# Performance work log

Hardware: AMD Instinct MI355X
Metric: run time of the kernel (lower is better)

The kernel has to match this reference:

```python
import jax, jax.numpy as jnp
import numpy as np

N = 100000      # nodes
E = 1600000     # edges (avg degree 16)
IN, H, EMB = 64, 128, 64
G = 64          # graphs in the batch


def _w(key, shape, fan_in):
    return jax.random.normal(key, shape, jnp.float32) * (1.0 / np.sqrt(fan_in))


def setup_inputs() -> dict:
    key = jax.random.key(0)
    ks = jax.random.split(key, 16)
    x = jax.random.normal(ks[0], (N, IN), jnp.float32)
    edge_index = jax.random.randint(ks[1], (2, E), 0, N, dtype=jnp.int64)
    batch = jnp.sort(jax.random.randint(ks[2], (N,), 0, G, dtype=jnp.int64))
    return {
        "x": x,
        "edge_index": edge_index,
        "batch": batch,
        # SAGEConv 1: lin_l acts on aggregated neighbors, lin_r on the root node
        "Wl1": _w(ks[3], (IN, H), IN), "Wr1": _w(ks[4], (IN, H), IN), "b1": jnp.zeros((H,), jnp.float32),
        "Wl2": _w(ks[5], (H, H), H), "Wr2": _w(ks[6], (H, H), H), "b2": jnp.zeros((H,), jnp.float32),
        "Wl3": _w(ks[7], (H, H), H), "Wr3": _w(ks[8], (H, H), H), "b3": jnp.zeros((H,), jnp.float32),
        "W_lin1": _w(ks[9], (H, H // 2), H), "b_lin1": jnp.zeros((H // 2,), jnp.float32),
        "W_lin2": _w(ks[10], (H // 2, EMB), H // 2), "b_lin2": jnp.zeros((EMB,), jnp.float32),
    }


def _sage_conv(x, src, dst, Wl, Wr, b):
    # mean-aggregate source features onto destination nodes
    msg_sum = jax.ops.segment_sum(x[src], dst, num_segments=N)          # [N, d]
    deg = jax.ops.segment_sum(jnp.ones((src.shape[0],), x.dtype), dst, num_segments=N)
    mean = msg_sum / jnp.clip(deg, 1.0)[:, None]
    return mean @ Wl + x @ Wr + b


def _forward(x, edge_index, batch,
             Wl1, Wr1, b1, Wl2, Wr2, b2, Wl3, Wr3, b3,
             W_lin1, b_lin1, W_lin2, b_lin2):
    src, dst = edge_index[0], edge_index[1]
    h = jax.nn.relu(_sage_conv(x, src, dst, Wl1, Wr1, b1))
    h = jax.nn.relu(_sage_conv(h, src, dst, Wl2, Wr2, b2))
    h = jax.nn.relu(_sage_conv(h, src, dst, Wl3, Wr3, b3))
    # global mean pool per graph
    pooled = jax.ops.segment_sum(h, batch, num_segments=G)              # [G, H]
    counts = jax.ops.segment_sum(jnp.ones((N,), h.dtype), batch, num_segments=G)
    pooled = pooled / jnp.clip(counts, 1.0)[:, None]
    h = jax.nn.relu(pooled @ W_lin1 + b_lin1)
    # dropout p=0.5 is identity in eval mode
    return h @ W_lin2 + b_lin2


def reference(x, edge_index, batch,
              Wl1, Wr1, b1, Wl2, Wr2, b2, Wl3, Wr3, b3,
              W_lin1, b_lin1, W_lin2, b_lin2):
    return _forward(x, edge_index, batch, Wl1, Wr1, b1, Wl2, Wr2, b2,
                    Wl3, Wr3, b3, W_lin1, b_lin1, W_lin2, b_lin2)
```

## Files before the change

kernel.cpp:

```cpp
#include <hip/hip_runtime.h>
#include <hip/hip_bf16.h>
#include <cstdint>
#include <cstddef>

#define NN 100000
#define NE 1600000
#define NG 64
#define NPAD 100096
#define NBUK 782
#define CAP 3072
#define NFB 256
#define CHUNK 6250

typedef short short8v __attribute__((ext_vector_type(8)));
typedef float float4v __attribute__((ext_vector_type(4)));


__device__ __forceinline__ int lower_bound_i(const int* __restrict__ a, int n, int v) {
  int lo = 0, hi = n;
  while (lo < hi) { int m = (lo + hi) >> 1; if (a[m] < v) lo = m + 1; else hi = m; }
  return lo;
}

__device__ __forceinline__ float bf2f(ushort u) {
  return __uint_as_float(((unsigned int)u) << 16);
}

__device__ __forceinline__ float bflo(unsigned int u) {
  return __uint_as_float(u << 16);
}
__device__ __forceinline__ float bfhi(unsigned int u) {
  return __uint_as_float(u & 0xffff0000u);
}

__device__ __forceinline__ ushort f2bf(float f) {
  __hip_bfloat16 h = __float2bfloat16(f);
  return *reinterpret_cast<ushort*>(&h);
}


__global__ void pack_x_kernel(const float* __restrict__ x, ushort* __restrict__ xb,
                              int* __restrict__ bcur) {
  int i4 = blockIdx.x * blockDim.x + threadIdx.x;
  if (i4 < NBUK) bcur[i4] = i4 * CAP;
  int idx = i4 * 4;
  if (idx >= NN * 64) return;
  float4 v = *(const float4*)(x + idx);
  ushort4 o;
  o.x = f2bf(v.x); o.y = f2bf(v.y); o.z = f2bf(v.z); o.w = f2bf(v.w);
  *(ushort4*)(xb + idx) = o;
}

__device__ __forceinline__ void pack_one(const float* __restrict__ Wl,
                                         const float* __restrict__ Wr,
                                         ushort* __restrict__ Wp, int K, int idx) {
  int lane = idx & 63;
  int ft   = (idx >> 6) & 7;
  int kkp  = idx >> 9;
  int kbase = kkp * 32 + (lane >> 4) * 8;
  int isR = kbase >= K;
  const float* W = isR ? Wr : Wl;
  int k0 = kbase - (isR ? K : 0);
  int colf = ft * 16 + (lane & 15);
  ushort4 lo, hi;
  lo.x = f2bf(W[(k0 + 0) * 128 + colf]);
  lo.y = f2bf(W[(k0 + 1) * 128 + colf]);
  lo.z = f2bf(W[(k0 + 2) * 128 + colf]);
  lo.w = f2bf(W[(k0 + 3) * 128 + colf]);
  hi.x = f2bf(W[(k0 + 4) * 128 + colf]);
  hi.y = f2bf(W[(k0 + 5) * 128 + colf]);
  hi.z = f2bf(W[(k0 + 6) * 128 + colf]);
  hi.w = f2bf(W[(k0 + 7) * 128 + colf]);
  *(ushort4*)(Wp + (size_t)idx * 8)     = lo;
  *(ushort4*)(Wp + (size_t)idx * 8 + 4) = hi;
}

__global__ void pack_w_all_kernel(const float* __restrict__ Wl1, const float* __restrict__ Wr1,
                                  ushort* __restrict__ wp1,
                                  const float* __restrict__ Wl2, const float* __restrict__ Wr2,
                                  ushort* __restrict__ wp2,
                                  const float* __restrict__ Wl3, const float* __restrict__ Wr3,
                                  ushort* __restrict__ wp3) {
  int idx = blockIdx.x * blockDim.x + threadIdx.x;
  if (idx < 2048)       pack_one(Wl1, Wr1, wp1, 64,  idx);
  else if (idx < 6144)  pack_one(Wl2, Wr2, wp2, 128, idx - 2048);
  else if (idx < 10240) pack_one(Wl3, Wr3, wp3, 128, idx - 6144);
}


__global__ __launch_bounds__(256) void bucket_fill_kernel(const int* __restrict__ src,
                                                          const int* __restrict__ dst,
                                                          int* __restrict__ bcur,
                                                          unsigned int* __restrict__ bp) {
  __shared__ int lhist[NBUK];
  __shared__ int lbase[NBUK];
  int tid = threadIdx.x;
  int e0 = blockIdx.x * CHUNK;
  int e1 = e0 + CHUNK;
  for (int i = tid; i < NBUK; i += 256) lhist[i] = 0;
  __syncthreads();
  for (int i = e0 + tid; i < e1; i += 256) atomicAdd(&lhist[dst[i] >> 7], 1);
  __syncthreads();
  for (int b = tid; b < NBUK; b += 256) {
    int c = lhist[b];
    lbase[b] = c ? atomicAdd(&bcur[b], c) : 0;
    lhist[b] = 0;
  }
  __syncthreads();
  for (int i = e0 + tid; i < e1; i += 256) {
    int d = dst[i];
    int b = d >> 7;
    int p = atomicAdd(&lhist[b], 1);
    int pos = lbase[b] + p;
    if (pos < (b + 1) * CAP)
      bp[pos] = ((unsigned int)(d & 127) << 17) | (unsigned int)src[i];
  }
}

__global__ __launch_bounds__(1024) void bucket_scan_kernel(const int* __restrict__ bcur,
                                                           int* __restrict__ boff,
                                                           int* __restrict__ rs,
                                                           float* __restrict__ pooled) {
  __shared__ int wsum[16];
  int tid = threadIdx.x, lane = tid & 63, wid = tid >> 6;
  int v = 0;
  if (tid < NBUK) v = min(bcur[tid] - tid * CAP, CAP);
  int incl = v;
  #pragma unroll
  for (int off = 1; off < 64; off <<= 1) {
    int t = __shfl_up(incl, off, 64);
    if (lane >= off) incl += t;
  }
  if (lane == 63) wsum[wid] = incl;
  __syncthreads();
  if (tid == 0) {
    int acc = 0;
    #pragma unroll
    for (int j = 0; j < 16; ++j) { int t = wsum[j]; wsum[j] = acc; acc += t; }
  }
  __syncthreads();
  int excl = incl - v + wsum[wid];
  if (tid <= NBUK) boff[tid] = excl;
  for (int i = tid; i < NG * 128; i += 1024) pooled[i] = 0.f;
  if (tid == 0) rs[NN] = NE;
}

__global__ __launch_bounds__(256) void bucket_csr_kernel(const unsigned int* __restrict__ bp,
                                                         const int* __restrict__ boff,
                                                         int* __restrict__ rs,
                                                         int* __restrict__ col) {
  __shared__ int sdeg[128], sinc[128], lcur[128];
  int b = blockIdx.x, tid = threadIdx.x;
  int n0 = b << 7;
  int e0 = boff[b], e1 = boff[b + 1];
  int cnt = e1 - e0;
  const unsigned int* __restrict__ mybp = bp + (size_t)b * CAP;
  if (tid < 128) sdeg[tid] = 0;
  __syncthreads();
  for (int i = tid; i < cnt; i += 256) atomicAdd(&sdeg[mybp[i] >> 17], 1);
  __syncthreads();
  if (tid < 128) sinc[tid] = sdeg[tid];
  __syncthreads();
  #pragma unroll
  for (int off = 1; off < 128; off <<= 1) {
    int add = 0;
    if (tid < 128 && tid >= off) add = sinc[tid - off];
    __syncthreads();
    if (tid < 128) sinc[tid] += add;
    __syncthreads();
  }
  if (tid < 128) {
    int excl = sinc[tid] - sdeg[tid];
    lcur[tid] = excl;
    int node = n0 + tid;
    if (node < NN) rs[node] = e0 + excl;
  }
  __syncthreads();
  for (int i = tid; i < cnt; i += 256) {
    unsigned int v = mybp[i];
    int p = atomicAdd(&lcur[v >> 17], 1);
    col[e0 + p] = (int)(v & 0x1FFFF);
  }
}


__global__ __launch_bounds__(256) void agg64_kernel(const unsigned int* __restrict__ X,
                                                    const int* __restrict__ rs,
                                                    const int* __restrict__ col,
                                                    unsigned int* __restrict__ out, int n) {
  int lane = threadIdx.x & 63;
  int node = blockIdx.x * 4 + (threadIdx.x >> 6);
  if (node >= n) return;
  int a = rs[node], b = rs[node + 1];
  int grp = lane >> 3, fl = lane & 7;
  float acc[8];
  #pragma unroll
  for (int j = 0; j < 8; ++j) acc[j] = 0.f;
  for (int jb = a; jb < b; jb += 64) {
    int v = (jb + lane < b) ? col[jb + lane] : 0;
    int cnt = min(64, b - jb);
    for (int t = 0; t < cnt; t += 8) {
      int idx = t + grp;
      int s = __shfl(v, min(idx, cnt - 1), 64);
      uint4 u = *(const uint4*)(X + (size_t)s * 32 + fl * 4);
      if (idx < cnt) {
        acc[0] += bflo(u.x); acc[1] += bfhi(u.x);
        acc[2] += bflo(u.y); acc[3] += bfhi(u.y);
        acc[4] += bflo(u.z); acc[5] += bfhi(u.z);
        acc[6] += bflo(u.w); acc[7] += bfhi(u.w);
      }
    }
  }
  #pragma unroll
  for (int off = 8; off <= 32; off <<= 1)
    #pragma unroll
    for (int j = 0; j < 8; ++j) acc[j] += __shfl_xor(acc[j], off, 64);
  int d = b - a;
  float inv = d > 0 ? 1.0f / (float)d : 0.f;
  if (grp == 0) {
    uint4 o;
    o.x = (unsigned int)f2bf(acc[0] * inv) | ((unsigned int)f2bf(acc[1] * inv) << 16);
    o.y = (unsigned int)f2bf(acc[2] * inv) | ((unsigned int)f2bf(acc[3] * inv) << 16);
    o.z = (unsigned int)f2bf(acc[4] * inv) | ((unsigned int)f2bf(acc[5] * inv) << 16);
    o.w = (unsigned int)f2bf(acc[6] * inv) | ((unsigned int)f2bf(acc[7] * inv) << 16);
    *(uint4*)(out + (size_t)node * 32 + fl * 4) = o;
  }
}

__global__ __launch_bounds__(256) void agg128_kernel(const unsigned int* __restrict__ X,
                                                     const int* __restrict__ rs,
                                                     const int* __restrict__ col,
                                                     unsigned int* __restrict__ out, int n) {
  int lane = threadIdx.x & 63;
  int node = blockIdx.x * 4 + (threadIdx.x >> 6);
  if (node >= n) return;
  int a = rs[node], b = rs[node + 1];
  int grp = lane >> 4, fl = lane & 15;
  float acc[8];
  #pragma unroll
  for (int j = 0; j < 8; ++j) acc[j] = 0.f;
  for (int jb = a; jb < b; jb += 64) {
    int v = (jb + lane < b) ? col[jb + lane] : 0;
    int cnt = min(64, b - jb);
    for (int t = 0; t < cnt; t += 4) {
      int idx = t + grp;
      int s = __shfl(v, min(idx, cnt - 1), 64);
      uint4 u = *(const uint4*)(X + (size_t)s * 64 + fl * 4);
      if (idx < cnt) {
        acc[0] += bflo(u.x); acc[1] += bfhi(u.x);
        acc[2] += bflo(u.y); acc[3] += bfhi(u.y);
        acc[4] += bflo(u.z); acc[5] += bfhi(u.z);
        acc[6] += bflo(u.w); acc[7] += bfhi(u.w);
      }
    }
  }
  #pragma unroll
  for (int off = 16; off <= 32; off <<= 1)
    #pragma unroll
    for (int j = 0; j < 8; ++j) acc[j] += __shfl_xor(acc[j], off, 64);
  int d = b - a;
  float inv = d > 0 ? 1.0f / (float)d : 0.f;
  if (grp == 0) {
    uint4 o;
    o.x = (unsigned int)f2bf(acc[0] * inv) | ((unsigned int)f2bf(acc[1] * inv) << 16);
    o.y = (unsigned int)f2bf(acc[2] * inv) | ((unsigned int)f2bf(acc[3] * inv) << 16);
    o.z = (unsigned int)f2bf(acc[4] * inv) | ((unsigned int)f2bf(acc[5] * inv) << 16);
    o.w = (unsigned int)f2bf(acc[6] * inv) | ((unsigned int)f2bf(acc[7] * inv) << 16);
    *(uint4*)(out + (size_t)node * 64 + fl * 4) = o;
  }
}


template <int K>
__global__ __launch_bounds__(256) void mfma_gemm_kernel(const ushort* __restrict__ Mean,
                                                        const ushort* __restrict__ Xb,
                                                        const ushort* __restrict__ Wp,
                                                        const float* __restrict__ bias,
                                                        ushort* __restrict__ Out) {
  constexpr int KS = K / 32;
  int lane = threadIdx.x & 63;
  int wave = threadIdx.x >> 6;
  int quad = lane >> 4;
  int l16  = lane & 15;
  size_t node0 = (size_t)blockIdx.x * 128 + wave * 32;

  float4v acc[2][8];
  #pragma unroll
  for (int g = 0; g < 2; ++g)
    #pragma unroll
    for (int ft = 0; ft < 8; ++ft)
      acc[g][ft] = (float4v){0.f, 0.f, 0.f, 0.f};

  #pragma unroll
  for (int s = 0; s < 2; ++s) {
    const ushort* __restrict__ A = s ? Xb : Mean;
    #pragma unroll
    for (int kk = 0; kk < KS; ++kk) {
      int kkp = s * KS + kk;
      short8v wv[8];
      const ushort* wb = Wp + ((size_t)(kkp * 8) * 64 + lane) * 8;
      #pragma unroll
      for (int ft = 0; ft < 8; ++ft)
        wv[ft] = *(const short8v*)(wb + (size_t)ft * 64 * 8);
      short8v av[2];
      #pragma unroll
      for (int g = 0; g < 2; ++g)
        av[g] = *(const short8v*)(A + (node0 + g * 16 + l16) * K + kk * 32 + quad * 8);
      #pragma unroll
      for (int g = 0; g < 2; ++g)
        #pragma unroll
        for (int ft = 0; ft < 8; ++ft)
          acc[g][ft] = __builtin_amdgcn_mfma_f32_16x16x32_bf16(wv[ft], av[g], acc[g][ft], 0, 0, 0);
    }
  }

  #pragma unroll
  for (int g = 0; g < 2; ++g) {
    size_t nrow = node0 + g * 16 + l16;
    #pragma unroll
    for (int ft = 0; ft < 8; ++ft) {
      float4 bb = *(const float4*)(bias + ft * 16 + quad * 4);
      float4v v = acc[g][ft];
      ushort4 o;
      o.x = f2bf(fmaxf(v.x + bb.x, 0.f));
      o.y = f2bf(fmaxf(v.y + bb.y, 0.f));
      o.z = f2bf(fmaxf(v.z + bb.z, 0.f));
      o.w = f2bf(fmaxf(v.w + bb.w, 0.f));
      *(ushort4*)(Out + nrow * 128 + ft * 16 + quad * 4) = o;
    }
  }
}


__global__ __launch_bounds__(256) void pool_kernel(const unsigned int* __restrict__ H,
                                                   const int* __restrict__ batch,
                                                   float* __restrict__ pooled) {
  __shared__ float part[4][128];
  int t = threadIdx.x;
  int fl = t & 15;
  int sub = t >> 4;
  int n0 = blockIdx.x * 128;
  for (int i = t; i < 512; i += 256) ((float*)part)[i] = 0.f;
  int g0 = batch[n0];
  __syncthreads();
  float acc[8];
  #pragma unroll
  for (int j = 0; j < 8; ++j) acc[j] = 0.f;
  int curgi = 0;
  for (int i = 0; i < 8; ++i) {
    int node = n0 + sub + 16 * i;
    if (node >= NN) break;
    int gi = batch[node] - g0;
    if (gi != curgi) {
      if (curgi < 4) {
        #pragma unroll
        for (int j = 0; j < 8; ++j) {
          if (acc[j] != 0.f) atomicAdd(&part[curgi][fl * 8 + j], acc[j]);
          acc[j] = 0.f;
        }
      }
      curgi = gi;
    }
    uint4 u = *(const uint4*)(H + (size_t)node * 64 + fl * 4);
    if (curgi < 4) {
      acc[0] += bflo(u.x); acc[1] += bfhi(u.x);
      acc[2] += bflo(u.y); acc[3] += bfhi(u.y);
      acc[4] += bflo(u.z); acc[5] += bfhi(u.z);
      acc[6] += bflo(u.w); acc[7] += bfhi(u.w);
    } else {
      float* pg = &pooled[(g0 + gi) * 128 + fl * 8];
      atomicAdd(&pg[0], bflo(u.x)); atomicAdd(&pg[1], bfhi(u.x));
      atomicAdd(&pg[2], bflo(u.y)); atomicAdd(&pg[3], bfhi(u.y));
      atomicAdd(&pg[4], bflo(u.z)); atomicAdd(&pg[5], bfhi(u.z));
      atomicAdd(&pg[6], bflo(u.w)); atomicAdd(&pg[7], bfhi(u.w));
    }
  }
  if (curgi < 4) {
    #pragma unroll
    for (int j = 0; j < 8; ++j)
      if (acc[j] != 0.f) atomicAdd(&part[curgi][fl * 8 + j], acc[j]);
  }
  __syncthreads();
  int nlast = min(n0 + 127, NN - 1);
  int nslot = min(batch[nlast] - g0 + 1, 4);
  if (t < 128) {
    for (int s = 0; s < nslot; ++s) {
      float v = part[s][t];
      if (v != 0.f) atomicAdd(&pooled[(g0 + s) * 128 + t], v);
    }
  }
}


__global__ __launch_bounds__(64) void mlp_kernel(const float* __restrict__ pooled,
                                                 const int* __restrict__ batch,
                                                 const float* __restrict__ W1,
                                                 const float* __restrict__ b1,
                                                 const float* __restrict__ W2,
                                                 const float* __restrict__ b2,
                                                 float* __restrict__ out, int n) {
  __shared__ float p[128];
  __shared__ float h1[64];
  int g = blockIdx.x, f = threadIdx.x;
  int lo = lower_bound_i(batch, n, g);
  int hi = lower_bound_i(batch, n, g + 1);
  float inv = (hi > lo) ? 1.0f / (float)(hi - lo) : 0.f;
  p[f]      = pooled[g * 128 + f] * inv;
  p[f + 64] = pooled[g * 128 + 64 + f] * inv;
  __syncthreads();
  float a = b1[f];
  #pragma unroll 8
  for (int k = 0; k < 128; ++k) a = fmaf(p[k], W1[k * 64 + f], a);
  a = fmaxf(a, 0.f);
  h1[f] = a;
  __syncthreads();
  float o = b2[f];
  #pragma unroll 8
  for (int k = 0; k < 64; ++k) o = fmaf(h1[k], W2[k * 64 + f], o);
  out[g * 64 + f] = o;
}


extern "C" void kernel_launch(void* const* d_in, const int* in_sizes, int n_in,
                              void* d_out, int out_size, void* d_ws, size_t ws_size,
                              hipStream_t stream) {
  const float* x      = (const float*)d_in[0];
  const int*   edge   = (const int*)d_in[1];
  const int*   batch  = (const int*)d_in[2];
  const float* Wl1    = (const float*)d_in[3];
  const float* Wr1    = (const float*)d_in[4];
  const float* b1     = (const float*)d_in[5];
  const float* Wl2    = (const float*)d_in[6];
  const float* Wr2    = (const float*)d_in[7];
  const float* b2     = (const float*)d_in[8];
  const float* Wl3    = (const float*)d_in[9];
  const float* Wr3    = (const float*)d_in[10];
  const float* b3     = (const float*)d_in[11];
  const float* Wlin1  = (const float*)d_in[12];
  const float* blin1  = (const float*)d_in[13];
  const float* Wlin2  = (const float*)d_in[14];
  const float* blin2  = (const float*)d_in[15];
  float* out = (float*)d_out;

  const int* src = edge;
  const int* dst = edge + NE;

  char* ws = (char*)d_ws;
  size_t off = 0;
  auto alloc = [&](size_t bytes) -> char* {
    char* p = ws + off;
    off = (off + bytes + 255) & ~(size_t)255;
    return p;
  };
  int*    rs     = (int*)alloc((size_t)(NN + 1) * 4);
  int*    col    = (int*)alloc((size_t)NE * 4);
  int*    bcur   = (int*)alloc((size_t)NBUK * 4);
  int*    boff   = (int*)alloc((size_t)(NBUK + 1) * 4);
  unsigned int* bp = (unsigned int*)alloc((size_t)NBUK * CAP * 4);
  ushort* xb     = (ushort*)alloc((size_t)NPAD * 64 * 2);
  ushort* mean64 = (ushort*)alloc((size_t)NPAD * 64 * 2);
  ushort* mean128= (ushort*)alloc((size_t)NPAD * 128 * 2);
  ushort* h1     = (ushort*)alloc((size_t)NPAD * 128 * 2);
  ushort* h2     = (ushort*)alloc((size_t)NPAD * 128 * 2);
  ushort* h3     = (ushort*)alloc((size_t)NPAD * 128 * 2);
  ushort* wp1    = (ushort*)alloc((size_t)2 * 64 * 128 * 2);
  ushort* wp2    = (ushort*)alloc((size_t)2 * 128 * 128 * 2);
  ushort* wp3    = (ushort*)alloc((size_t)2 * 128 * 128 * 2);
  float*  pooled = (float*)alloc((size_t)NG * 128 * 4);
  (void)ws_size; (void)n_in; (void)in_sizes; (void)out_size;

  pack_x_kernel<<<(NN * 64 / 4 + 255) / 256, 256, 0, stream>>>(x, xb, bcur);
  pack_w_all_kernel<<<40, 256, 0, stream>>>(Wl1, Wr1, wp1, Wl2, Wr2, wp2, Wl3, Wr3, wp3);
  bucket_fill_kernel<<<NFB, 256, 0, stream>>>(src, dst, bcur, bp);
  bucket_scan_kernel<<<1, 1024, 0, stream>>>(bcur, boff, rs, pooled);
  bucket_csr_kernel<<<NBUK, 256, 0, stream>>>(bp, boff, rs, col);

  agg64_kernel<<<(NN + 3) / 4, 256, 0, stream>>>((const unsigned int*)xb, rs, col,
                                                 (unsigned int*)mean64, NN);
  mfma_gemm_kernel<64><<<NPAD / 128, 256, 0, stream>>>(mean64, xb, wp1, b1, h1);

  agg128_kernel<<<(NN + 3) / 4, 256, 0, stream>>>((const unsigned int*)h1, rs, col,
                                                  (unsigned int*)mean128, NN);
  mfma_gemm_kernel<128><<<NPAD / 128, 256, 0, stream>>>(mean128, h1, wp2, b2, h2);

  agg128_kernel<<<(NN + 3) / 4, 256, 0, stream>>>((const unsigned int*)h2, rs, col,
                                                  (unsigned int*)mean128, NN);
  mfma_gemm_kernel<128><<<NPAD / 128, 256, 0, stream>>>(mean128, h2, wp3, b3, h3);

  pool_kernel<<<(NN + 127) / 128, 256, 0, stream>>>((const unsigned int*)h3, batch, pooled);
  mlp_kernel<<<NG, 64, 0, stream>>>(pooled, batch, Wlin1, blin1, Wlin2, blin2, out, NN);
}
```

Before: 412.7 us.

## Split neighbor aggregation by feature chunk with per-thread serial gathers

Replaces the wave-per-node aggregation kernels with one templated kernel. Each block handles a 512-node tile for a single 16-byte-per-thread feature chunk (8 bf16 columns across a thread pair), and each thread walks its nodes' edge lists serially with a prefetched column index. The aim is to shrink the working set of each gather pass so it stays cache-resident, and to drop the shuffle and reduction overhead. In exchange the column index list is re-read once per chunk, and per-thread serial loops leave little memory-level parallelism and are sensitive to uneven degrees. Index loads and output stores are marked nontemporal.

```diff
diff --git a/kernel.cpp b/kernel.cpp
--- a/kernel.cpp
+++ b/kernel.cpp
@@ -11,9 +11,11 @@
 #define CAP 3072
 #define NFB 256
 #define CHUNK 6250
+#define AGGT 196
 
 typedef short short8v __attribute__((ext_vector_type(8)));
 typedef float float4v __attribute__((ext_vector_type(4)));
+typedef unsigned int uint4v __attribute__((ext_vector_type(4)));
 
 
 __device__ __forceinline__ int lower_bound_i(const int* __restrict__ a, int n, int v) {
@@ -184,89 +186,44 @@
 }
 
 
-__global__ __launch_bounds__(256) void agg64_kernel(const unsigned int* __restrict__ X,
-                                                    const int* __restrict__ rs,
-                                                    const int* __restrict__ col,
-                                                    unsigned int* __restrict__ out, int n) {
-  int lane = threadIdx.x & 63;
-  int node = blockIdx.x * 4 + (threadIdx.x >> 6);
-  if (node >= n) return;
-  int a = rs[node], b = rs[node + 1];
-  int grp = lane >> 3, fl = lane & 7;
-  float acc[8];
-  #pragma unroll
-  for (int j = 0; j < 8; ++j) acc[j] = 0.f;
-  for (int jb = a; jb < b; jb += 64) {
-    int v = (jb + lane < b) ? col[jb + lane] : 0;
-    int cnt = min(64, b - jb);
-    for (int t = 0; t < cnt; t += 8) {
-      int idx = t + grp;
-      int s = __shfl(v, min(idx, cnt - 1), 64);
-      uint4 u = *(const uint4*)(X + (size_t)s * 32 + fl * 4);
-      if (idx < cnt) {
-        acc[0] += bflo(u.x); acc[1] += bfhi(u.x);
-        acc[2] += bflo(u.y); acc[3] += bfhi(u.y);
-        acc[4] += bflo(u.z); acc[5] += bfhi(u.z);
-        acc[6] += bflo(u.w); acc[7] += bfhi(u.w);
-      }
-    }
-  }
-  #pragma unroll
-  for (int off = 8; off <= 32; off <<= 1)
-    #pragma unroll
-    for (int j = 0; j < 8; ++j) acc[j] += __shfl_xor(acc[j], off, 64);
-  int d = b - a;
-  float inv = d > 0 ? 1.0f / (float)d : 0.f;
-  if (grp == 0) {
-    uint4 o;
-    o.x = (unsigned int)f2bf(acc[0] * inv) | ((unsigned int)f2bf(acc[1] * inv) << 16);
-    o.y = (unsigned int)f2bf(acc[2] * inv) | ((unsigned int)f2bf(acc[3] * inv) << 16);
-    o.z = (unsigned int)f2bf(acc[4] * inv) | ((unsigned int)f2bf(acc[5] * inv) << 16);
-    o.w = (unsigned int)f2bf(acc[6] * inv) | ((unsigned int)f2bf(acc[7] * inv) << 16);
-    *(uint4*)(out + (size_t)node * 32 + fl * 4) = o;
-  }
-}
-
-__global__ __launch_bounds__(256) void agg128_kernel(const unsigned int* __restrict__ X,
-                                                     const int* __restrict__ rs,
-                                                     const int* __restrict__ col,
-                                                     unsigned int* __restrict__ out, int n) {
-  int lane = threadIdx.x & 63;
-  int node = blockIdx.x * 4 + (threadIdx.x >> 6);
-  if (node >= n) return;
-  int a = rs[node], b = rs[node + 1];
-  int grp = lane >> 4, fl = lane & 15;
-  float acc[8];
-  #pragma unroll
-  for (int j = 0; j < 8; ++j) acc[j] = 0.f;
-  for (int jb = a; jb < b; jb += 64) {
-    int v = (jb + lane < b) ? col[jb + lane] : 0;
-    int cnt = min(64, b - jb);
-    for (int t = 0; t < cnt; t += 4) {
-      int idx = t + grp;
-      int s = __shfl(v, min(idx, cnt - 1), 64);
-      uint4 u = *(const uint4*)(X + (size_t)s * 64 + fl * 4);
-      if (idx < cnt) {
-        acc[0] += bflo(u.x); acc[1] += bfhi(u.x);
-        acc[2] += bflo(u.y); acc[3] += bfhi(u.y);
-        acc[4] += bflo(u.z); acc[5] += bfhi(u.z);
-        acc[6] += bflo(u.w); acc[7] += bfhi(u.w);
-      }
-    }
-  }
-  #pragma unroll
-  for (int off = 16; off <= 32; off <<= 1)
-    #pragma unroll
-    for (int j = 0; j < 8; ++j) acc[j] += __shfl_xor(acc[j], off, 64);
-  int d = b - a;
-  float inv = d > 0 ? 1.0f / (float)d : 0.f;
-  if (grp == 0) {
-    uint4 o;
-    o.x = (unsigned int)f2bf(acc[0] * inv) | ((unsigned int)f2bf(acc[1] * inv) << 16);
-    o.y = (unsigned int)f2bf(acc[2] * inv) | ((unsigned int)f2bf(acc[3] * inv) << 16);
-    o.z = (unsigned int)f2bf(acc[4] * inv) | ((unsigned int)f2bf(acc[5] * inv) << 16);
-    o.w = (unsigned int)f2bf(acc[6] * inv) | ((unsigned int)f2bf(acc[7] * inv) << 16);
-    *(uint4*)(out + (size_t)node * 64 + fl * 4) = o;
+template <int ROWU, int NCH>
+__global__ __launch_bounds__(256) void aggc_kernel(const unsigned int* __restrict__ X,
+                                                   const int* __restrict__ rs,
+                                                   const int* __restrict__ col,
+                                                   unsigned int* __restrict__ out) {
+  int tid = threadIdx.x;
+  int chunk = blockIdx.x & (NCH - 1);
+  int tile  = blockIdx.x / NCH;
+  int p   = tid & 1;
+  int grp = tid >> 1;
+  int node0 = tile * 512 + grp * 4;
+  int off = chunk * 8 + p * 4;
+  const unsigned int* __restrict__ Xc = X + off;
+  #pragma unroll
+  for (int i = 0; i < 4; ++i) {
+    int node = node0 + i;
+    if (node >= NN) break;
+    int a = rs[node], b = rs[node + 1];
+    float a0 = 0.f, a1 = 0.f, a2 = 0.f, a3 = 0.f;
+    float a4 = 0.f, a5 = 0.f, a6 = 0.f, a7 = 0.f;
+    int sn = (a < b) ? __builtin_nontemporal_load(col + a) : 0;
+    for (int j = a; j < b; ++j) {
+      int s = sn;
+      if (j + 1 < b) sn = __builtin_nontemporal_load(col + j + 1);
+      uint4v u = *(const uint4v*)(Xc + (size_t)s * ROWU);
+      a0 += bflo(u.x); a1 += bfhi(u.x);
+      a2 += bflo(u.y); a3 += bfhi(u.y);
+      a4 += bflo(u.z); a5 += bfhi(u.z);
+      a6 += bflo(u.w); a7 += bfhi(u.w);
+    }
+    int d = b - a;
+    float inv = d > 0 ? 1.0f / (float)d : 0.f;
+    uint4v o;
+    o.x = (unsigned int)f2bf(a0 * inv) | ((unsigned int)f2bf(a1 * inv) << 16);
+    o.y = (unsigned int)f2bf(a2 * inv) | ((unsigned int)f2bf(a3 * inv) << 16);
+    o.z = (unsigned int)f2bf(a4 * inv) | ((unsigned int)f2bf(a5 * inv) << 16);
+    o.w = (unsigned int)f2bf(a6 * inv) | ((unsigned int)f2bf(a7 * inv) << 16);
+    __builtin_nontemporal_store(o, (uint4v*)(out + (size_t)node * ROWU + off));
   }
 }
 
@@ -475,16 +432,16 @@
   bucket_scan_kernel<<<1, 1024, 0, stream>>>(bcur, boff, rs, pooled);
   bucket_csr_kernel<<<NBUK, 256, 0, stream>>>(bp, boff, rs, col);
 
-  agg64_kernel<<<(NN + 3) / 4, 256, 0, stream>>>((const unsigned int*)xb, rs, col,
-                                                 (unsigned int*)mean64, NN);
+  aggc_kernel<32, 4><<<AGGT * 4, 256, 0, stream>>>((const unsigned int*)xb, rs, col,
+                                                   (unsigned int*)mean64);
   mfma_gemm_kernel<64><<<NPAD / 128, 256, 0, stream>>>(mean64, xb, wp1, b1, h1);
 
-  agg128_kernel<<<(NN + 3) / 4, 256, 0, stream>>>((const unsigned int*)h1, rs, col,
-                                                  (unsigned int*)mean128, NN);
+  aggc_kernel<64, 8><<<AGGT * 8, 256, 0, stream>>>((const unsigned int*)h1, rs, col,
+                                                   (unsigned int*)mean128);
   mfma_gemm_kernel<128><<<NPAD / 128, 256, 0, stream>>>(mean128, h1, wp2, b2, h2);
 
-  agg128_kernel<<<(NN + 3) / 4, 256, 0, stream>>>((const unsigned int*)h2, rs, col,
-                                                  (unsigned int*)mean128, NN);
+  aggc_kernel<64, 8><<<AGGT * 8, 256, 0, stream>>>((const unsigned int*)h2, rs, col,
+                                                   (unsigned int*)mean128);
   mfma_gemm_kernel<128><<<NPAD / 128, 256, 0, stream>>>(mean128, h2, wp3, b3, h3);
 
   pool_kernel<<<(NN + 127) / 128, 256, 0, stream>>>((const unsigned int*)h3, batch, pooled);
```

Result: slower. 1.313 ms (+218.2%).

## Gather neighbor features in fp8 copies to halve aggregation bandwidth

Applied to the files above, without the earlier changes.

Each GEMM epilogue and the input pack kernel now also write an fp8 (e4m3) copy of the node features. The three mean-aggregation kernels gather that copy instead of bf16, halving the bytes moved per random neighbor read. The agg128 lane mapping becomes 8 lanes per row with 16 accumulators, and output stores become scattered 4-byte writes. The trade is precision: fp8 carries about 3 mantissa bits, which may exceed tolerance, and the extra fp8 writes add some traffic.

```diff
diff --git a/kernel.cpp b/kernel.cpp
--- a/kernel.cpp
+++ b/kernel.cpp
@@ -14,6 +14,7 @@
 
 typedef short short8v __attribute__((ext_vector_type(8)));
 typedef float float4v __attribute__((ext_vector_type(4)));
+typedef float float2v __attribute__((ext_vector_type(2)));
 
 
 __device__ __forceinline__ int lower_bound_i(const int* __restrict__ a, int n, int v) {
@@ -38,9 +39,14 @@
   return *reinterpret_cast<ushort*>(&h);
 }
 
+template <bool HI>
+__device__ __forceinline__ unsigned int pk_fp8(float a, float b, unsigned int old) {
+  return (unsigned int)__builtin_amdgcn_cvt_pk_fp8_f32(a, b, (int)old, HI);
+}
+
 
 __global__ void pack_x_kernel(const float* __restrict__ x, ushort* __restrict__ xb,
-                              int* __restrict__ bcur) {
+                              unsigned int* __restrict__ x8, int* __restrict__ bcur) {
   int i4 = blockIdx.x * blockDim.x + threadIdx.x;
   if (i4 < NBUK) bcur[i4] = i4 * CAP;
   int idx = i4 * 4;
@@ -49,6 +55,9 @@
   ushort4 o;
   o.x = f2bf(v.x); o.y = f2bf(v.y); o.z = f2bf(v.z); o.w = f2bf(v.w);
   *(ushort4*)(xb + idx) = o;
+  unsigned int r = pk_fp8<false>(v.x, v.y, 0u);
+  r = pk_fp8<true>(v.z, v.w, r);
+  x8[i4] = r;
 }
 
 __device__ __forceinline__ void pack_one(const float* __restrict__ Wl,
@@ -184,7 +193,7 @@
 }
 
 
-__global__ __launch_bounds__(256) void agg64_kernel(const unsigned int* __restrict__ X,
+__global__ __launch_bounds__(256) void agg64_kernel(const unsigned int* __restrict__ X8,
                                                     const int* __restrict__ rs,
                                                     const int* __restrict__ col,
                                                     unsigned int* __restrict__ out, int n) {
@@ -202,12 +211,14 @@
     for (int t = 0; t < cnt; t += 8) {
       int idx = t + grp;
       int s = __shfl(v, min(idx, cnt - 1), 64);
-      uint4 u = *(const uint4*)(X + (size_t)s * 32 + fl * 4);
+      uint2 u = *(const uint2*)(X8 + (size_t)s * 16 + fl * 2);
       if (idx < cnt) {
-        acc[0] += bflo(u.x); acc[1] += bfhi(u.x);
-        acc[2] += bflo(u.y); acc[3] += bfhi(u.y);
-        acc[4] += bflo(u.z); acc[5] += bfhi(u.z);
-        acc[6] += bflo(u.w); acc[7] += bfhi(u.w);
+        float2v p0 = __builtin_amdgcn_cvt_pk_f32_fp8(u.x, false);
+        float2v p1 = __builtin_amdgcn_cvt_pk_f32_fp8(u.x, true);
+        float2v p2 = __builtin_amdgcn_cvt_pk_f32_fp8(u.y, false);
+        float2v p3 = __builtin_amdgcn_cvt_pk_f32_fp8(u.y, true);
+        acc[0] += p0.x; acc[1] += p0.y; acc[2] += p1.x; acc[3] += p1.y;
+        acc[4] += p2.x; acc[5] += p2.y; acc[6] += p3.x; acc[7] += p3.y;
       }
     }
   }
@@ -217,17 +228,14 @@
     for (int j = 0; j < 8; ++j) acc[j] += __shfl_xor(acc[j], off, 64);
   int d = b - a;
   float inv = d > 0 ? 1.0f / (float)d : 0.f;
-  if (grp == 0) {
-    uint4 o;
-    o.x = (unsigned int)f2bf(acc[0] * inv) | ((unsigned int)f2bf(acc[1] * inv) << 16);
-    o.y = (unsigned int)f2bf(acc[2] * inv) | ((unsigned int)f2bf(acc[3] * inv) << 16);
-    o.z = (unsigned int)f2bf(acc[4] * inv) | ((unsigned int)f2bf(acc[5] * inv) << 16);
-    o.w = (unsigned int)f2bf(acc[6] * inv) | ((unsigned int)f2bf(acc[7] * inv) << 16);
-    *(uint4*)(out + (size_t)node * 32 + fl * 4) = o;
-  }
-}
-
-__global__ __launch_bounds__(256) void agg128_kernel(const unsigned int* __restrict__ X,
+  if (grp < 4) {
+    unsigned int o = (unsigned int)f2bf(acc[2 * grp] * inv) |
+                     ((unsigned int)f2bf(acc[2 * grp + 1] * inv) << 16);
+    out[(size_t)node * 32 + fl * 4 + grp] = o;
+  }
+}
+
+__global__ __launch_bounds__(256) void agg128_kernel(const unsigned int* __restrict__ X8,
                                                      const int* __restrict__ rs,
                                                      const int* __restrict__ col,
                                                      unsigned int* __restrict__ out, int n) {
@@ -235,39 +243,42 @@
   int node = blockIdx.x * 4 + (threadIdx.x >> 6);
   if (node >= n) return;
   int a = rs[node], b = rs[node + 1];
-  int grp = lane >> 4, fl = lane & 15;
-  float acc[8];
-  #pragma unroll
-  for (int j = 0; j < 8; ++j) acc[j] = 0.f;
+  int grp = lane >> 3, fl = lane & 7;
+  float acc[16];
+  #pragma unroll
+  for (int j = 0; j < 16; ++j) acc[j] = 0.f;
   for (int jb = a; jb < b; jb += 64) {
     int v = (jb + lane < b) ? col[jb + lane] : 0;
     int cnt = min(64, b - jb);
-    for (int t = 0; t < cnt; t += 4) {
+    for (int t = 0; t < cnt; t += 8) {
       int idx = t + grp;
       int s = __shfl(v, min(idx, cnt - 1), 64);
-      uint4 u = *(const uint4*)(X + (size_t)s * 64 + fl * 4);
+      uint4 u = *(const uint4*)(X8 + (size_t)s * 32 + fl * 4);
       if (idx < cnt) {
-        acc[0] += bflo(u.x); acc[1] += bfhi(u.x);
-        acc[2] += bflo(u.y); acc[3] += bfhi(u.y);
-        acc[4] += bflo(u.z); acc[5] += bfhi(u.z);
-        acc[6] += bflo(u.w); acc[7] += bfhi(u.w);
+        float2v p0 = __builtin_amdgcn_cvt_pk_f32_fp8(u.x, false);
+        float2v p1 = __builtin_amdgcn_cvt_pk_f32_fp8(u.x, true);
+        float2v p2 = __builtin_amdgcn_cvt_pk_f32_fp8(u.y, false);
+        float2v p3 = __builtin_amdgcn_cvt_pk_f32_fp8(u.y, true);
+        acc[0] += p0.x; acc[1] += p0.y; acc[2] += p1.x; acc[3] += p1.y;
+        acc[4] += p2.x; acc[5] += p2.y; acc[6] += p3.x; acc[7] += p3.y;
+        float2v p4 = __builtin_amdgcn_cvt_pk_f32_fp8(u.z, false);
+        float2v p5 = __builtin_amdgcn_cvt_pk_f32_fp8(u.z, true);
+        float2v p6 = __builtin_amdgcn_cvt_pk_f32_fp8(u.w, false);
+        float2v p7 = __builtin_amdgcn_cvt_pk_f32_fp8(u.w, true);
+        acc[8]  += p4.x; acc[9]  += p4.y; acc[10] += p5.x; acc[11] += p5.y;
+        acc[12] += p6.x; acc[13] += p6.y; acc[14] += p7.x; acc[15] += p7.y;
       }
     }
   }
   #pragma unroll
-  for (int off = 16; off <= 32; off <<= 1)
-    #pragma unroll
-    for (int j = 0; j < 8; ++j) acc[j] += __shfl_xor(acc[j], off, 64);
+  for (int off = 8; off <= 32; off <<= 1)
+    #pragma unroll
+    for (int j = 0; j < 16; ++j) acc[j] += __shfl_xor(acc[j], off, 64);
   int d = b - a;
   float inv = d > 0 ? 1.0f / (float)d : 0.f;
-  if (grp == 0) {
-    uint4 o;
-    o.x = (unsigned int)f2bf(acc[0] * inv) | ((unsigned int)f2bf(acc[1] * inv) << 16);
-    o.y = (unsigned int)f2bf(acc[2] * inv) | ((unsigned int)f2bf(acc[3] * inv) << 16);
-    o.z = (unsigned int)f2bf(acc[4] * inv) | ((unsigned int)f2bf(acc[5] * inv) << 16);
-    o.w = (unsigned int)f2bf(acc[6] * inv) | ((unsigned int)f2bf(acc[7] * inv) << 16);
-    *(uint4*)(out + (size_t)node * 64 + fl * 4) = o;
-  }
+  unsigned int o = (unsigned int)f2bf(acc[2 * grp] * inv) |
+                   ((unsigned int)f2bf(acc[2 * grp + 1] * inv) << 16);
+  out[(size_t)node * 64 + fl * 8 + grp] = o;
 }
 
 
@@ -276,7 +287,8 @@
                                                         const ushort* __restrict__ Xb,
                                                         const ushort* __restrict__ Wp,
                                                         const float* __restrict__ bias,
-                                                        ushort* __restrict__ Out) {
+                                                        ushort* __restrict__ Out,
+                                                        unsigned int* __restrict__ Out8) {
   constexpr int KS = K / 32;
   int lane = threadIdx.x & 63;
   int wave = threadIdx.x >> 6;
@@ -321,12 +333,18 @@
     for (int ft = 0; ft < 8; ++ft) {
       float4 bb = *(const float4*)(bias + ft * 16 + quad * 4);
       float4v v = acc[g][ft];
+      float r0 = fmaxf(v.x + bb.x, 0.f);
+      float r1 = fmaxf(v.y + bb.y, 0.f);
+      float r2 = fmaxf(v.z + bb.z, 0.f);
+      float r3 = fmaxf(v.w + bb.w, 0.f);
       ushort4 o;
-      o.x = f2bf(fmaxf(v.x + bb.x, 0.f));
-      o.y = f2bf(fmaxf(v.y + bb.y, 0.f));
-      o.z = f2bf(fmaxf(v.z + bb.z, 0.f));
-      o.w = f2bf(fmaxf(v.w + bb.w, 0.f));
+      o.x = f2bf(r0); o.y = f2bf(r1); o.z = f2bf(r2); o.w = f2bf(r3);
       *(ushort4*)(Out + nrow * 128 + ft * 16 + quad * 4) = o;
+      if (Out8) {
+        unsigned int r = pk_fp8<false>(r0, r1, 0u);
+        r = pk_fp8<true>(r2, r3, r);
+        Out8[nrow * 32 + ft * 4 + quad] = r;
+      }
     }
   }
 }
@@ -458,6 +476,8 @@
   int*    boff   = (int*)alloc((size_t)(NBUK + 1) * 4);
   unsigned int* bp = (unsigned int*)alloc((size_t)NBUK * CAP * 4);
   ushort* xb     = (ushort*)alloc((size_t)NPAD * 64 * 2);
+  unsigned int* x8 = (unsigned int*)alloc((size_t)NPAD * 64);
+  unsigned int* h8 = (unsigned int*)alloc((size_t)NPAD * 128);
   ushort* mean64 = (ushort*)alloc((size_t)NPAD * 64 * 2);
   ushort* mean128= (ushort*)alloc((size_t)NPAD * 128 * 2);
   ushort* h1     = (ushort*)alloc((size_t)NPAD * 128 * 2);
@@ -469,23 +489,20 @@
   float*  pooled = (float*)alloc((size_t)NG * 128 * 4);
   (void)ws_size; (void)n_in; (void)in_sizes; (void)out_size;
 
-  pack_x_kernel<<<(NN * 64 / 4 + 255) / 256, 256, 0, stream>>>(x, xb, bcur);
+  pack_x_kernel<<<(NN * 64 / 4 + 255) / 256, 256, 0, stream>>>(x, xb, x8, bcur);
   pack_w_all_kernel<<<40, 256, 0, stream>>>(Wl1, Wr1, wp1, Wl2, Wr2, wp2, Wl3, Wr3, wp3);
   bucket_fill_kernel<<<NFB, 256, 0, stream>>>(src, dst, bcur, bp);
   bucket_scan_kernel<<<1, 1024, 0, stream>>>(bcur, boff, rs, pooled);
   bucket_csr_kernel<<<NBUK, 256, 0, stream>>>(bp, boff, rs, col);
 
-  agg64_kernel<<<(NN + 3) / 4, 256, 0, stream>>>((const unsigned int*)xb, rs, col,
-                                                 (unsigned int*)mean64, NN);
-  mfma_gemm_kernel<64><<<NPAD / 128, 256, 0, stream>>>(mean64, xb, wp1, b1, h1);
-
-  agg128_kernel<<<(NN + 3) / 4, 256, 0, stream>>>((const unsigned int*)h1, rs, col,
-                                                  (unsigned int*)mean128, NN);
-  mfma_gemm_kernel<128><<<NPAD / 128, 256, 0, stream>>>(mean128, h1, wp2, b2, h2);
-
-  agg128_kernel<<<(NN + 3) / 4, 256, 0, stream>>>((const unsigned int*)h2, rs, col,
-                                                  (unsigned int*)mean128, NN);
-  mfma_gemm_kernel<128><<<NPAD / 128, 256, 0, stream>>>(mean128, h2, wp3, b3, h3);
+  agg64_kernel<<<(NN + 3) / 4, 256, 0, stream>>>(x8, rs, col, (unsigned int*)mean64, NN);
+  mfma_gemm_kernel<64><<<NPAD / 128, 256, 0, stream>>>(mean64, xb, wp1, b1, h1, h8);
+
+  agg128_kernel<<<(NN + 3) / 4, 256, 0, stream>>>(h8, rs, col, (unsigned int*)mean128, NN);
+  mfma_gemm_kernel<128><<<NPAD / 128, 256, 0, stream>>>(mean128, h1, wp2, b2, h2, h8);
+
+  agg128_kernel<<<(NN + 3) / 4, 256, 0, stream>>>(h8, rs, col, (unsigned int*)mean128, NN);
+  mfma_gemm_kernel<128><<<NPAD / 128, 256, 0, stream>>>(mean128, h2, wp3, b3, h3, nullptr);
 
   pool_kernel<<<(NN + 127) / 128, 256, 0, stream>>>((const unsigned int*)h3, batch, pooled);
   mlp_kernel<<<NG, 64, 0, stream>>>(pooled, batch, Wlin1, blin1, Wlin2, blin2, out, NN);
```

Result: slower. 431.5 us (+4.6%).
